# Kernel optimization log

Hardware: AMD Instinct MI355X
Metric: run time of the kernel (lower is better)

The kernel has to match this reference:

```python
import jax, jax.numpy as jnp
import numpy as np

N_NODES = 200000
N_EDGES = 200000
N_GRAPHS = 128
IN_FEATS, HID_FEATS, OUT_FEATS = 256, 128, 128


def gcn_conv(x, W, b, src, dst, n_nodes):
    """PyG-style GCNConv: add self-loops, symmetric deg^-1/2 normalization."""
    h = x @ W  # [N, out]
    # degree with self-loops: deg[i] = 1 + (# edges with target i)
    deg = 1.0 + jax.ops.segment_sum(jnp.ones(src.shape[0], x.dtype), dst,
                                    num_segments=n_nodes)
    dinv = jax.lax.rsqrt(deg)
    norm = dinv[src] * dinv[dst]  # per-edge coeff
    agg = jax.ops.segment_sum(h[src] * norm[:, None], dst, num_segments=n_nodes)
    agg = agg + h * (1.0 / deg)[:, None]  # self-loop contribution
    return agg + b


def setup_inputs() -> dict:
    key = jax.random.key(0)
    k = jax.random.split(key, 8)
    x = jax.random.normal(k[0], (N_NODES, IN_FEATS), jnp.float32)
    edge_index = jax.random.randint(k[1], (2, N_EDGES), 0, N_NODES)
    batch = jnp.sort(jax.random.randint(k[2], (N_NODES,), 0, N_GRAPHS))
    root_index = jax.random.randint(k[3], (N_GRAPHS,), 0, N_NODES)
    # GCNConv params (xavier-ish scale)
    W1 = jax.random.normal(k[4], (IN_FEATS, HID_FEATS), jnp.float32) * (2.0 / (IN_FEATS + HID_FEATS)) ** 0.5
    b1 = jnp.zeros((HID_FEATS,), jnp.float32)
    W2 = jax.random.normal(k[5], (HID_FEATS + IN_FEATS, OUT_FEATS), jnp.float32) * (2.0 / (HID_FEATS + IN_FEATS + OUT_FEATS)) ** 0.5
    b2 = jnp.zeros((OUT_FEATS,), jnp.float32)
    return {"x": x, "edge_index": edge_index, "batch": batch,
            "root_index": root_index, "W1": W1, "b1": b1, "W2": W2, "b2": b2}


def reference(x, edge_index, batch, root_index, W1, b1, W2, b2):
    src, dst = edge_index[0], edge_index[1]
    x1 = x  # raw input features
    h = gcn_conv(x, W1, b1, src, dst, N_NODES)  # conv1 -> [N, hid]
    x2 = h
    # root broadcast: root_extend[i] = x1[root_index[batch[i]]]
    root_extend = x1[root_index[batch]]  # [N, in]
    h = jnp.concatenate([h, root_extend], axis=1)  # [N, hid+in]
    h = jax.nn.relu(h)
    # F.dropout(training=self.training): eval mode -> identity
    h = gcn_conv(h, W2, b2, src, dst, N_NODES)  # conv2 -> [N, out]
    h = jax.nn.relu(h)
    root_extend2 = x2[root_index[batch]]  # [N, hid]
    h = jnp.concatenate([h, root_extend2], axis=1)  # [N, out+hid]
    # scatter_mean over graphs
    sums = jax.ops.segment_sum(h, batch, num_segments=N_GRAPHS)
    counts = jax.ops.segment_sum(jnp.ones((N_NODES,), h.dtype), batch,
                                 num_segments=N_GRAPHS)
    return sums / jnp.maximum(counts, 1.0)[:, None]  # [B, out+hid]
```

## Files before the change

### kernel.cpp

```cpp
#include <hip/hip_runtime.h>
#include <stddef.h>

constexpr int N_NODES = 200000;
constexpr int N_EDGES = 200000;
constexpr int N_GRAPHS = 128;
constexpr int IN_F = 256;
constexpr int HID_F = 128;
constexpr int OUT_F = 128;
constexpr int OUT_W = OUT_F + HID_F;
constexpr int SCAN_NB = (N_NODES + 1023) / 1024;
constexpr int EDGE_NB = (N_EDGES + 255) / 256;
constexpr int CHUNKS = 128;

typedef __attribute__((ext_vector_type(8))) short short8;
typedef __attribute__((ext_vector_type(4))) float float4v;

__device__ __forceinline__ short f2bf(float f) {
    union { float f; unsigned u; } v; v.f = f;
    unsigned r = v.u + 0x7fffu + ((v.u >> 16) & 1u);
    return (short)(r >> 16);
}
__device__ __forceinline__ float bf2f(unsigned short s) {
    union { unsigned u; float f; } v; v.u = ((unsigned)s) << 16;
    return v.f;
}

__global__ __launch_bounds__(256) void init_kernel(
    const int* __restrict__ batch, const float* __restrict__ W1,
    const float* __restrict__ W2,
    int* __restrict__ cursor, float* __restrict__ rootlin,
    int* __restrict__ startv, int* __restrict__ cntg,
    short* __restrict__ Bt1, short* __restrict__ Bt2)
{
    __shared__ int s_start[N_GRAPHS + 1];
    const int t = threadIdx.x;
    const int gid = blockIdx.x * 256 + t;

    if (gid < N_NODES) cursor[gid] = 0;
    if (gid < N_GRAPHS * OUT_F) rootlin[gid] = 0.f;
    if (gid < 128 * IN_F) {
        int n = gid >> 8, k = gid & 255;
        Bt1[(size_t)n * IN_F + k] = f2bf(W1[(size_t)k * 128 + n]);
    } else if (gid < 128 * IN_F + 128 * HID_F) {
        int tw = gid - 128 * IN_F;
        int n = tw >> 7, k = tw & 127;
        Bt2[(size_t)n * HID_F + k] = f2bf(W2[(size_t)k * 128 + n]);
    }
    if (blockIdx.x == 0) {
        if (t <= N_GRAPHS) {
            int g = t, lo = 0, hi = N_NODES;
            while (lo < hi) {
                int mid = (lo + hi) >> 1;
                if (batch[mid] < g) lo = mid + 1; else hi = mid;
            }
            s_start[t] = lo;
        }
        __syncthreads();
        if (t < N_GRAPHS) {
            startv[t] = s_start[t];
            cntg[t] = s_start[t + 1] - s_start[t];
        }
    }
}

__global__ void edge_prep_kernel(const int* __restrict__ dst, int* __restrict__ cntin, int E) {
    int e = blockIdx.x * blockDim.x + threadIdx.x;
    if (e < E) atomicAdd(&cntin[dst[e]], 1);
}

__global__ __launch_bounds__(1024) void scan_reduce_kernel(const int* __restrict__ cnt,
                                                           int* __restrict__ partial, int n) {
    __shared__ int sm[1024];
    int t = threadIdx.x;
    int i = blockIdx.x * 1024 + t;
    sm[t] = (i < n) ? cnt[i] : 0;
    __syncthreads();
    for (int ofs = 512; ofs > 0; ofs >>= 1) {
        if (t < ofs) sm[t] += sm[t + ofs];
        __syncthreads();
    }
    if (t == 0) partial[blockIdx.x] = sm[0];
}

__global__ void scan_base_kernel(int* __restrict__ partial, int nb) {
    __shared__ int sm[256];
    int t = threadIdx.x;
    sm[t] = (t < nb) ? partial[t] : 0;
    __syncthreads();
    for (int ofs = 1; ofs < 256; ofs <<= 1) {
        int v = (t >= ofs) ? sm[t - ofs] : 0;
        __syncthreads();
        sm[t] += v;
        __syncthreads();
    }
    if (t < nb) partial[t] = (t == 0) ? 0 : sm[t - 1];
}

__global__ __launch_bounds__(1024) void scan_final_kernel(const int* __restrict__ cnt,
                                                          const int* __restrict__ partial,
                                                          int* __restrict__ rp,
                                                          int* __restrict__ cur,
                                                          float* __restrict__ dinv, int n) {
    __shared__ int sm[1024];
    int t = threadIdx.x;
    int i = blockIdx.x * 1024 + t;
    int v = (i < n) ? cnt[i] : 0;
    sm[t] = v;
    __syncthreads();
    for (int ofs = 1; ofs < 1024; ofs <<= 1) {
        int u = (t >= ofs) ? sm[t - ofs] : 0;
        __syncthreads();
        sm[t] += u;
        __syncthreads();
    }
    int base = partial[blockIdx.x];
    if (i < n) {
        int ex = base + sm[t] - v;
        rp[i] = ex;
        cur[i] = ex;
        dinv[i] = rsqrtf(1.0f + (float)v);
        if (i == n - 1) rp[n] = ex + v;
    }
}

__global__ __launch_bounds__(256) void bucket_rootlin_kernel(
    const int* __restrict__ src, const int* __restrict__ dst,
    int* __restrict__ cur, int* __restrict__ adj,
    const float* __restrict__ x, const int* __restrict__ root_index,
    const float* __restrict__ W2, float* __restrict__ rootlin)
{
    int b = blockIdx.x;
    int t = threadIdx.x;
    if (b < EDGE_NB) {
        int e = b * 256 + t;
        if (e < N_EDGES) {
            int pos = atomicAdd(&cur[dst[e]], 1);
            adj[pos] = src[e];
        }
    } else {
        int rb = b - EDGE_NB;
        int g = rb >> 1;
        int f = t & 127;
        int k0 = (rb & 1) * 128 + (t >> 7) * 64;
        int r = root_index[g];
        const float* xr = x + (size_t)r * IN_F;
        float acc = 0.f;
        for (int k = k0; k < k0 + 64; ++k)
            acc += fmaxf(xr[k], 0.f) * W2[(size_t)(HID_F + k) * OUT_F + f];
        atomicAdd(&rootlin[(size_t)g * OUT_F + f], acc);
    }
}

__global__ __launch_bounds__(256) void agg2_kernel(
    const unsigned short* __restrict__ hs1, const float* __restrict__ dinv,
    const float* __restrict__ b1v, const int* __restrict__ rp,
    const int* __restrict__ adj, unsigned short* __restrict__ hsag)
{
    int gid = blockIdx.x * 256 + threadIdx.x;
    int r = gid >> 3;
    int c0 = (gid & 7) * 16;
    const unsigned short* hp = hs1 + (size_t)r * 128 + c0;
    float sum[16];
    {
        short8 h0 = *(const short8*)hp;
        short8 h1 = *(const short8*)(hp + 8);
        #pragma unroll
        for (int q = 0; q < 8; ++q) {
            sum[q] = bf2f((unsigned short)h0[q]);
            sum[8 + q] = bf2f((unsigned short)h1[q]);
        }
    }
    int e0 = rp[r], e1 = rp[r + 1];
    for (int e = e0; e < e1; ++e) {
        const unsigned short* qp = hs1 + (size_t)adj[e] * 128 + c0;
        short8 h0 = *(const short8*)qp;
        short8 h1 = *(const short8*)(qp + 8);
        #pragma unroll
        for (int q = 0; q < 8; ++q) {
            sum[q] += bf2f((unsigned short)h0[q]);
            sum[8 + q] += bf2f((unsigned short)h1[q]);
        }
    }
    float di = dinv[r];
    short8 s0, s1;
    #pragma unroll
    for (int q = 0; q < 8; ++q) {
        s0[q] = f2bf(fmaxf(di * sum[q] + b1v[c0 + q], 0.f));
        s1[q] = f2bf(fmaxf(di * sum[8 + q] + b1v[c0 + 8 + q], 0.f));
    }
    unsigned short* op = hsag + (size_t)r * 128 + c0;
    *(short8*)op = s0;
    *(short8*)(op + 8) = s1;
}

template<int KTOT, bool ABF16, bool ADDROOT>
__global__ __launch_bounds__(256) void mfma_gemm_kernel(
    const void* __restrict__ Ap, const short* __restrict__ Bt,
    unsigned short* __restrict__ outp,
    const float* __restrict__ dinv,
    const float* __restrict__ rootlin, const int* __restrict__ batch)
{
    __shared__ __align__(16) short As[64][136];
    __shared__ __align__(16) short Bs[128][136];

    const int tid = threadIdx.x;
    const int wave = tid >> 6;
    const int lane = tid & 63;
    const int quad = lane >> 4;
    const int l16  = lane & 15;
    const int row0 = blockIdx.x * 64;

    float4v acc[8];
    #pragma unroll
    for (int c = 0; c < 8; ++c) acc[c] = (float4v){0.f, 0.f, 0.f, 0.f};

    const int arow = tid >> 2;
    const int ac8 = (tid & 3) * 8;
    const int bn = tid >> 1;
    const int bk = (tid & 1) * 64;

    for (int kb = 0; kb < KTOT / 128; ++kb) {
        {
            const short* bp = Bt + (size_t)bn * KTOT + kb * 128 + bk;
            #pragma unroll
            for (int j = 0; j < 8; ++j)
                *(short8*)&Bs[bn][bk + 8 * j] = *(const short8*)(bp + 8 * j);
        }
        if (ABF16) {
            const unsigned short* A = (const unsigned short*)Ap;
            const unsigned short* ap = A + (size_t)(row0 + arow) * KTOT + kb * 128 + ac8;
            #pragma unroll
            for (int jj = 0; jj < 4; ++jj)
                *(short8*)&As[arow][ac8 + 32 * jj] = *(const short8*)(ap + 32 * jj);
        } else {
            const float* A = (const float*)Ap;
            const float* ap = A + (size_t)(row0 + arow) * KTOT + kb * 128 + ac8;
            #pragma unroll
            for (int jj = 0; jj < 4; ++jj) {
                float4 f0 = *(const float4*)(ap + 32 * jj);
                float4 f1 = *(const float4*)(ap + 32 * jj + 4);
                short8 s;
                s[0] = f2bf(f0.x); s[1] = f2bf(f0.y); s[2] = f2bf(f0.z); s[3] = f2bf(f0.w);
                s[4] = f2bf(f1.x); s[5] = f2bf(f1.y); s[6] = f2bf(f1.z); s[7] = f2bf(f1.w);
                *(short8*)&As[arow][ac8 + 32 * jj] = s;
            }
        }
        __syncthreads();
        #pragma unroll
        for (int ks = 0; ks < 4; ++ks) {
            short8 af = *(const short8*)&As[wave * 16 + l16][ks * 32 + quad * 8];
            #pragma unroll
            for (int c = 0; c < 8; ++c) {
                short8 bf = *(const short8*)&Bs[c * 16 + l16][ks * 32 + quad * 8];
                acc[c] = __builtin_amdgcn_mfma_f32_16x16x32_bf16(af, bf, acc[c], 0, 0, 0);
            }
        }
        __syncthreads();
    }

    #pragma unroll
    for (int r = 0; r < 4; ++r) {
        int row = row0 + wave * 16 + quad * 4 + r;
        float di = dinv[row];
        const float* rl = nullptr;
        if (ADDROOT) rl = rootlin + (size_t)batch[row] * 128;
        #pragma unroll
        for (int c = 0; c < 8; ++c) {
            int col = c * 16 + l16;
            float v = acc[c][r];
            if (ADDROOT) v += rl[col];
            outp[(size_t)row * 128 + col] = (unsigned short)f2bf(v * di);
        }
    }
}

__global__ void mean_kernel(const unsigned short* __restrict__ hs2,
                            const unsigned short* __restrict__ hs1,
                            const float* __restrict__ dinv, const float* __restrict__ b1v,
                            const float* __restrict__ b2v, const int* __restrict__ root_index,
                            const int* __restrict__ cnt, const int* __restrict__ start,
                            const int* __restrict__ rp, const int* __restrict__ adj,
                            float* __restrict__ pmean, float* __restrict__ out)
{
    int g = blockIdx.x;
    int c = blockIdx.y;
    int f = threadIdx.x;
    int s = start[g], n = cnt[g];
    int per = (n + CHUNKS - 1) / CHUNKS;
    int lo = s + c * per;
    int hi = min(s + n, lo + per);
    float bb = b2v[f];
    float accv = 0.f;
    for (int i = lo; i < hi; ++i) {
        float v = bf2f(hs2[(size_t)i * 128 + f]);
        int e0 = rp[i], e1 = rp[i + 1];
        for (int e = e0; e < e1; ++e)
            v += bf2f(hs2[(size_t)adj[e] * 128 + f]);
        accv += fmaxf(dinv[i] * v + bb, 0.f);
    }
    pmean[(size_t)c * (N_GRAPHS * 128) + g * 128 + f] = accv;
    if (c == 0) {
        int r = root_index[g];
        float v = 0.f;
        if (n > 0) {
            v = bf2f(hs1[(size_t)r * 128 + f]);
            int e0 = rp[r], e1 = rp[r + 1];
            for (int e = e0; e < e1; ++e)
                v += bf2f(hs1[(size_t)adj[e] * 128 + f]);
            v = dinv[r] * v + b1v[f];
        }
        out[(size_t)g * OUT_W + HID_F + f] = v;
    }
}

__global__ void meanreduce_kernel(const float* __restrict__ pmean,
                                  const int* __restrict__ cnt,
                                  float* __restrict__ out)
{
    int g = blockIdx.x;
    int f = threadIdx.x;
    float s = 0.f;
    for (int c = 0; c < CHUNKS; ++c)
        s += pmean[(size_t)c * (N_GRAPHS * 128) + g * 128 + f];
    out[(size_t)g * OUT_W + f] = s / (float)max(cnt[g], 1);
}


static inline size_t align_up(size_t x, size_t a) { return (x + a - 1) / a * a; }

extern "C" void kernel_launch(void* const* d_in, const int* in_sizes, int n_in,
                              void* d_out, int out_size, void* d_ws, size_t ws_size,
                              hipStream_t stream) {
    const float* x = (const float*)d_in[0];
    const int* ei = (const int*)d_in[1];
    const int* batch = (const int*)d_in[2];
    const int* root = (const int*)d_in[3];
    const float* W1 = (const float*)d_in[4];
    const float* b1 = (const float*)d_in[5];
    const float* W2 = (const float*)d_in[6];
    const float* b2 = (const float*)d_in[7];
    float* out = (float*)d_out;

    const int* src = ei;
    const int* dst = ei + N_EDGES;

    char* ws = (char*)d_ws;
    size_t off = 0;
    const size_t NB16 = (size_t)N_NODES * 128 * sizeof(unsigned short);

    float* dinv = (float*)(ws + off);    off = align_up(off + (size_t)N_NODES * sizeof(float), 256);
    int* cntg = (int*)(ws + off);        off = align_up(off + N_GRAPHS * sizeof(int), 256);
    int* startv = (int*)(ws + off);      off = align_up(off + N_GRAPHS * sizeof(int), 256);
    float* rootlin = (float*)(ws + off); off = align_up(off + (size_t)N_GRAPHS * OUT_F * sizeof(float), 256);
    short* Bt1 = (short*)(ws + off);     off = align_up(off + (size_t)128 * IN_F * sizeof(short), 256);
    short* Bt2 = (short*)(ws + off);     off = align_up(off + (size_t)128 * HID_F * sizeof(short), 256);
    int* rowptr = (int*)(ws + off);      off = align_up(off + (size_t)(N_NODES + 1) * sizeof(int), 256);
    int* cursor = (int*)(ws + off);      off = align_up(off + (size_t)N_NODES * sizeof(int), 256);
    int* partial = (int*)(ws + off);     off = align_up(off + (size_t)SCAN_NB * sizeof(int), 256);
    int* adj = (int*)(ws + off);         off = align_up(off + (size_t)N_EDGES * sizeof(int), 256);
    float* pmean = (float*)(ws + off);   off = align_up(off + (size_t)CHUNKS * N_GRAPHS * 128 * sizeof(float), 256);
    unsigned short* hs1 = (unsigned short*)(ws + off);  off = align_up(off + NB16, 256);
    unsigned short* hs2 = (unsigned short*)(ws + off);  off = align_up(off + NB16, 256);
    unsigned short* hsag = (unsigned short*)(ws + off); off = align_up(off + NB16, 256);
    (void)ws_size; (void)n_in; (void)in_sizes; (void)out_size;

    init_kernel<<<EDGE_NB, 256, 0, stream>>>(batch, W1, W2, cursor, rootlin,
                                             startv, cntg, Bt1, Bt2);
    edge_prep_kernel<<<EDGE_NB, 256, 0, stream>>>(dst, cursor, N_EDGES);
    scan_reduce_kernel<<<SCAN_NB, 1024, 0, stream>>>(cursor, partial, N_NODES);
    scan_base_kernel<<<1, 256, 0, stream>>>(partial, SCAN_NB);
    scan_final_kernel<<<SCAN_NB, 1024, 0, stream>>>(cursor, partial, rowptr, cursor, dinv, N_NODES);
    bucket_rootlin_kernel<<<EDGE_NB + 2 * N_GRAPHS, 256, 0, stream>>>(
        src, dst, cursor, adj, x, root, W2, rootlin);

    mfma_gemm_kernel<IN_F, false, false><<<N_NODES / 64, 256, 0, stream>>>(
        x, Bt1, hs1, dinv, nullptr, nullptr);

    agg2_kernel<<<(N_NODES * 8) / 256, 256, 0, stream>>>(hs1, dinv, b1, rowptr, adj, hsag);

    mfma_gemm_kernel<HID_F, true, true><<<N_NODES / 64, 256, 0, stream>>>(
        hsag, Bt2, hs2, dinv, rootlin, batch);

    dim3 mg(N_GRAPHS, CHUNKS);
    mean_kernel<<<mg, 128, 0, stream>>>(hs2, hs1, dinv, b1, b2, root, cntg, startv,
                                        rowptr, adj, pmean, out);
    meanreduce_kernel<<<N_GRAPHS, 128, 0, stream>>>(pmean, cntg, out);
}
```

Before: 476.3 us.

## Fuse neighbor aggregation into second GEMM and read weights directly from global

Removes the standalone aggregation kernel. The second GEMM's A-tile load now gathers neighbor rows from hs1 via CSR, applies dinv, bias and relu, and writes straight into shared memory. This drops the hsag intermediate write and read and one launch. The B-tile shared staging is also removed so MFMA operands load from global/L2, and the launch bounds now request higher occupancy, which may add global traffic for the weight matrix. The trailing sync of the last k-block is skipped.

```diff
diff --git a/kernel.cpp b/kernel.cpp
--- a/kernel.cpp
+++ b/kernel.cpp
@@ -151,57 +151,15 @@
     }
 }
 
-__global__ __launch_bounds__(256) void agg2_kernel(
-    const unsigned short* __restrict__ hs1, const float* __restrict__ dinv,
-    const float* __restrict__ b1v, const int* __restrict__ rp,
-    const int* __restrict__ adj, unsigned short* __restrict__ hsag)
-{
-    int gid = blockIdx.x * 256 + threadIdx.x;
-    int r = gid >> 3;
-    int c0 = (gid & 7) * 16;
-    const unsigned short* hp = hs1 + (size_t)r * 128 + c0;
-    float sum[16];
-    {
-        short8 h0 = *(const short8*)hp;
-        short8 h1 = *(const short8*)(hp + 8);
-        #pragma unroll
-        for (int q = 0; q < 8; ++q) {
-            sum[q] = bf2f((unsigned short)h0[q]);
-            sum[8 + q] = bf2f((unsigned short)h1[q]);
-        }
-    }
-    int e0 = rp[r], e1 = rp[r + 1];
-    for (int e = e0; e < e1; ++e) {
-        const unsigned short* qp = hs1 + (size_t)adj[e] * 128 + c0;
-        short8 h0 = *(const short8*)qp;
-        short8 h1 = *(const short8*)(qp + 8);
-        #pragma unroll
-        for (int q = 0; q < 8; ++q) {
-            sum[q] += bf2f((unsigned short)h0[q]);
-            sum[8 + q] += bf2f((unsigned short)h1[q]);
-        }
-    }
-    float di = dinv[r];
-    short8 s0, s1;
-    #pragma unroll
-    for (int q = 0; q < 8; ++q) {
-        s0[q] = f2bf(fmaxf(di * sum[q] + b1v[c0 + q], 0.f));
-        s1[q] = f2bf(fmaxf(di * sum[8 + q] + b1v[c0 + 8 + q], 0.f));
-    }
-    unsigned short* op = hsag + (size_t)r * 128 + c0;
-    *(short8*)op = s0;
-    *(short8*)(op + 8) = s1;
-}
-
-template<int KTOT, bool ABF16, bool ADDROOT>
-__global__ __launch_bounds__(256) void mfma_gemm_kernel(
+template<int KTOT, bool GATHER, bool ADDROOT>
+__global__ __launch_bounds__(256, 4) void mfma_gemm_kernel(
     const void* __restrict__ Ap, const short* __restrict__ Bt,
     unsigned short* __restrict__ outp,
-    const float* __restrict__ dinv,
-    const float* __restrict__ rootlin, const int* __restrict__ batch)
+    const float* __restrict__ dinv, const float* __restrict__ bvec,
+    const float* __restrict__ rootlin, const int* __restrict__ batch,
+    const int* __restrict__ rp, const int* __restrict__ adj)
 {
     __shared__ __align__(16) short As[64][136];
-    __shared__ __align__(16) short Bs[128][136];
 
     const int tid = threadIdx.x;
     const int wave = tid >> 6;
@@ -216,22 +174,40 @@
 
     const int arow = tid >> 2;
     const int ac8 = (tid & 3) * 8;
-    const int bn = tid >> 1;
-    const int bk = (tid & 1) * 64;
-
-    for (int kb = 0; kb < KTOT / 128; ++kb) {
-        {
-            const short* bp = Bt + (size_t)bn * KTOT + kb * 128 + bk;
+    constexpr int NKB = KTOT / 128;
+
+    for (int kb = 0; kb < NKB; ++kb) {
+        if (GATHER) {
+            const unsigned short* A = (const unsigned short*)Ap;
+            const int row = row0 + arow;
+            float sum[4][8];
+            const unsigned short* hp = A + (size_t)row * 128 + ac8;
             #pragma unroll
-            for (int j = 0; j < 8; ++j)
-                *(short8*)&Bs[bn][bk + 8 * j] = *(const short8*)(bp + 8 * j);
-        }
-        if (ABF16) {
-            const unsigned short* A = (const unsigned short*)Ap;
-            const unsigned short* ap = A + (size_t)(row0 + arow) * KTOT + kb * 128 + ac8;
+            for (int jj = 0; jj < 4; ++jj) {
+                short8 h = *(const short8*)(hp + 32 * jj);
+                #pragma unroll
+                for (int q = 0; q < 8; ++q) sum[jj][q] = bf2f((unsigned short)h[q]);
+            }
+            int e0 = rp[row], e1 = rp[row + 1];
+            for (int e = e0; e < e1; ++e) {
+                const unsigned short* qp = A + (size_t)adj[e] * 128 + ac8;
+                #pragma unroll
+                for (int jj = 0; jj < 4; ++jj) {
+                    short8 h = *(const short8*)(qp + 32 * jj);
+                    #pragma unroll
+                    for (int q = 0; q < 8; ++q) sum[jj][q] += bf2f((unsigned short)h[q]);
+                }
+            }
+            float asc = dinv[row];
             #pragma unroll
-            for (int jj = 0; jj < 4; ++jj)
-                *(short8*)&As[arow][ac8 + 32 * jj] = *(const short8*)(ap + 32 * jj);
+            for (int jj = 0; jj < 4; ++jj) {
+                const float* bv = bvec + ac8 + 32 * jj;
+                short8 s;
+                #pragma unroll
+                for (int q = 0; q < 8; ++q)
+                    s[q] = f2bf(fmaxf(asc * sum[jj][q] + bv[q], 0.f));
+                *(short8*)&As[arow][ac8 + 32 * jj] = s;
+            }
         } else {
             const float* A = (const float*)Ap;
             const float* ap = A + (size_t)(row0 + arow) * KTOT + kb * 128 + ac8;
@@ -249,13 +225,14 @@
         #pragma unroll
         for (int ks = 0; ks < 4; ++ks) {
             short8 af = *(const short8*)&As[wave * 16 + l16][ks * 32 + quad * 8];
+            const short* bbase = Bt + kb * 128 + ks * 32 + quad * 8;
             #pragma unroll
             for (int c = 0; c < 8; ++c) {
-                short8 bf = *(const short8*)&Bs[c * 16 + l16][ks * 32 + quad * 8];
+                short8 bf = *(const short8*)(bbase + (c * 16 + l16) * KTOT);
                 acc[c] = __builtin_amdgcn_mfma_f32_16x16x32_bf16(af, bf, acc[c], 0, 0, 0);
             }
         }
-        __syncthreads();
+        if (kb + 1 < NKB) __syncthreads();
     }
 
     #pragma unroll
@@ -361,7 +338,6 @@
     float* pmean = (float*)(ws + off);   off = align_up(off + (size_t)CHUNKS * N_GRAPHS * 128 * sizeof(float), 256);
     unsigned short* hs1 = (unsigned short*)(ws + off);  off = align_up(off + NB16, 256);
     unsigned short* hs2 = (unsigned short*)(ws + off);  off = align_up(off + NB16, 256);
-    unsigned short* hsag = (unsigned short*)(ws + off); off = align_up(off + NB16, 256);
     (void)ws_size; (void)n_in; (void)in_sizes; (void)out_size;
 
     init_kernel<<<EDGE_NB, 256, 0, stream>>>(batch, W1, W2, cursor, rootlin,
@@ -374,12 +350,10 @@
         src, dst, cursor, adj, x, root, W2, rootlin);
 
     mfma_gemm_kernel<IN_F, false, false><<<N_NODES / 64, 256, 0, stream>>>(
-        x, Bt1, hs1, dinv, nullptr, nullptr);
-
-    agg2_kernel<<<(N_NODES * 8) / 256, 256, 0, stream>>>(hs1, dinv, b1, rowptr, adj, hsag);
+        x, Bt1, hs1, dinv, nullptr, nullptr, nullptr, nullptr, nullptr);
 
     mfma_gemm_kernel<HID_F, true, true><<<N_NODES / 64, 256, 0, stream>>>(
-        hsag, Bt2, hs2, dinv, rootlin, batch);
+        hs1, Bt2, hs2, dinv, b1, rootlin, batch, rowptr, adj);
 
     dim3 mg(N_GRAPHS, CHUNKS);
     mean_kernel<<<mg, 128, 0, stream>>>(hs2, hs1, dinv, b1, b2, root, cntg, startv,
```

Measured after the change: 540.8 us. +13.6%, slower.
